# Optimization experiments

Measured on AMD Instinct MI355X. Metric: run time of the kernel, lower is better.

## Reference

```python
import jax, jax.numpy as jnp
import numpy as np

T, B, E, H, F = 1024, 2, 1024, 16, 8
D = E // H
R = 2 * T - 1  # relative positions T-1 .. -(T-1)


def setup_inputs() -> dict:
    key = jax.random.key(0)
    ks = jax.random.split(key, 11)
    std = float(np.sqrt(2.0 / (E + E)))
    return {
        "input": jax.random.normal(ks[0], (T, B, E), jnp.float32),
        "pos": jax.random.normal(ks[1], (R, B, E), jnp.float32),
        "factor": jax.random.normal(ks[2], (F,), jnp.float32),
        "in_proj_weight": jax.random.normal(ks[3], (3 * E * E, F), jnp.float32) * std,
        "pos_proj_weight": jax.random.normal(ks[4], (E * E, F), jnp.float32) * std,
        "out_proj_weight": jax.random.normal(ks[5], (E * E, F), jnp.float32) * std,
        "in_proj_bias": jax.random.normal(ks[6], (3 * E, F), jnp.float32) * 0.02,
        "pos_proj_bias": jax.random.normal(ks[7], (E, F), jnp.float32) * 0.02,
        "out_proj_bias": jax.random.normal(ks[8], (E, F), jnp.float32) * 0.02,
        "r_w_bias": jax.random.normal(ks[9], (E, F), jnp.float32) * 0.02,
        "r_r_bias": jax.random.normal(ks[10], (E, F), jnp.float32) * 0.02,
    }


def _rel_shift(x):
    # x: [BH, T, R] -> out[b, i, j] = x[b, i, j + (T-1) - i]
    bh, q, r = x.shape
    zp = jnp.zeros((bh, q, 1), x.dtype)
    xp = jnp.concatenate([zp, x], axis=2).reshape(bh, r + 1, q)
    return xp[:, 1:, :].reshape(bh, q, r)


def reference(input, pos, factor, in_proj_weight, pos_proj_weight, out_proj_weight,
              in_proj_bias, pos_proj_bias, out_proj_bias, r_w_bias, r_r_bias):
    # hypernetwork: generate effective weights from factor vector (torch.mv)
    W_in = (in_proj_weight @ factor).reshape(3 * E, E)
    W_pos = (pos_proj_weight @ factor).reshape(E, E)
    W_out = (out_proj_weight @ factor).reshape(E, E)
    b_in = in_proj_bias @ factor
    b_pos = pos_proj_bias @ factor
    b_out = out_proj_bias @ factor
    rw = (r_w_bias @ factor).reshape(H, D)  # content bias
    rr = (r_r_bias @ factor).reshape(H, D)  # position bias

    qkv = input @ W_in.T + b_in                      # [T, B, 3E]
    q, k, v = jnp.split(qkv, 3, axis=-1)
    q = q.reshape(T, B, H, D)
    k = k.reshape(T, B, H, D)
    v = v.reshape(T, B, H, D)
    r = (pos @ W_pos.T + b_pos).reshape(R, B, H, D)  # [R, B, H, D]

    scale = 1.0 / np.sqrt(D)
    # AC: content-content + content bias term
    AC = jnp.einsum('ibhd,jbhd->bhij', q + rw, k)    # [B, H, T, T]
    # BD: content-position + position bias term, then relative shift
    BD = jnp.einsum('ibhd,rbhd->bhir', q + rr, r)    # [B, H, T, R]
    BD = _rel_shift(BD.reshape(B * H, T, R))[:, :, :T].reshape(B, H, T, T)

    attn = jax.nn.softmax((AC + BD) * scale, axis=-1)  # [B, H, T, T]
    out = jnp.einsum('bhij,jbhd->ibhd', attn, v).reshape(T, B, E)
    out = out @ W_out.T + b_out                       # [T, B, E]
    return out
```

## Files before the change

kernel.cpp:

```cpp
#include <hip/hip_runtime.h>


typedef _Float16 h16;
typedef _Float16 h16x8 __attribute__((ext_vector_type(8)));
typedef _Float16 h16x4 __attribute__((ext_vector_type(4)));
typedef float f32x4 __attribute__((ext_vector_type(4)));

static __device__ __forceinline__ f32x4 mfma16(h16x8 a, h16x8 b, f32x4 c) {
  return __builtin_amdgcn_mfma_f32_16x16x32_f16(a, b, c, 0, 0, 0);
}
static __device__ __forceinline__ void gload16(const void* g, void* l) {
  __builtin_amdgcn_global_load_lds((const __attribute__((address_space(1))) void*)g,
                                   (__attribute__((address_space(3))) void*)l, 16, 0, 0);
}

__global__ __launch_bounds__(256) void hypernet_kernel(
    const float* __restrict__ fac,
    const float* __restrict__ w_in, const float* __restrict__ w_pos,
    const float* __restrict__ w_out, const float* __restrict__ b_in_w,
    const float* __restrict__ b_pos_w, const float* __restrict__ b_out_w,
    const float* __restrict__ rw_w, const float* __restrict__ rr_w,
    h16* __restrict__ Win, h16* __restrict__ Wpos, h16* __restrict__ Wout,
    float* __restrict__ bin, float* __restrict__ bpos, float* __restrict__ bout,
    float* __restrict__ rw, float* __restrict__ rr, h16* __restrict__ rb,
    const float* __restrict__ input, h16* __restrict__ in_h,
    const float* __restrict__ pos, h16* __restrict__ pos_h)
{
  float f0=fac[0],f1=fac[1],f2=fac[2],f3=fac[3],f4=fac[4],f5=fac[5],f6=fac[6],f7=fac[7];
#define DOT8(p) ((p)[0]*f0+(p)[1]*f1+(p)[2]*f2+(p)[3]*f3+(p)[4]*f4+(p)[5]*f5+(p)[6]*f6+(p)[7]*f7)
  if (blockIdx.x < 5120) {
    const int lane = threadIdx.x & 63;
    const int gw = blockIdx.x * 4 + (threadIdx.x >> 6);
    size_t rowBase = (size_t)gw * 256;
    const float* srcp; h16* dstp; size_t lr;
    if (rowBase < 3145728)      { srcp = w_in;  dstp = Win;  lr = rowBase; }
    else if (rowBase < 4194304) { srcp = w_pos; dstp = Wpos; lr = rowBase - 3145728; }
    else                        { srcp = w_out; dstp = Wout; lr = rowBase - 4194304; }
    const f32x4* p = reinterpret_cast<const f32x4*>(srcp) + lr*2;
    const int pi = (lane < 32) ? (lane << 1) : (((lane - 32) << 1) | 1);
    const float fa = (lane < 32) ? f0 : f4;
    const float fb = (lane < 32) ? f1 : f5;
    const float fc = (lane < 32) ? f2 : f6;
    const float fd = (lane < 32) ? f3 : f7;
    f32x4 v[8];
#pragma unroll
    for (int u = 0; u < 8; ++u) v[u] = p[(size_t)u*64 + pi];
    float full[8];
#pragma unroll
    for (int u = 0; u < 8; ++u) {
      float part = v[u].x*fa + v[u].y*fb + v[u].z*fc + v[u].w*fd;
      full[u] = part + __shfl_xor(part, 32, 64);
    }
    if (lane < 32) {
#pragma unroll
      for (int u = 0; u < 8; ++u)
        dstp[lr + u*32 + lane] = (h16)full[u];
    }
    return;
  }
  int idx = (blockIdx.x - 5120) * 256 + threadIdx.x;
  if (idx < 3072) { bin[idx]  = DOT8(b_in_w  + (size_t)idx*8); return; }
  idx -= 3072;
  if (idx < 1024) { bpos[idx] = DOT8(b_pos_w + (size_t)idx*8); return; }
  idx -= 1024;
  if (idx < 1024) { bout[idx] = DOT8(b_out_w + (size_t)idx*8); return; }
  idx -= 1024;
  if (idx < 1024) { rw[idx]   = DOT8(rw_w    + (size_t)idx*8); return; }
  idx -= 1024;
  if (idx < 1024) { rr[idx]   = DOT8(rr_w    + (size_t)idx*8); return; }
  idx -= 1024;
  if (idx < 2048) { rb[(((size_t)(idx >> 6)) << 17) + 2047*64 + (idx & 63)] = (h16)0.f; return; }
  idx -= 2048;
  if (idx < 262144) {
    const float4* ip = reinterpret_cast<const float4*>(input) + (size_t)idx*2;
    float4 a = ip[0], b = ip[1];
    h16x8 o = { (h16)a.x, (h16)a.y, (h16)a.z, (h16)a.w,
                (h16)b.x, (h16)b.y, (h16)b.z, (h16)b.w };
    reinterpret_cast<h16x8*>(in_h)[idx] = o;
    return;
  }
  idx -= 262144;
  if (idx < 524032) {
    const float4* pp = reinterpret_cast<const float4*>(pos) + (size_t)idx*2;
    float4 a = pp[0], b = pp[1];
    h16x8 o = { (h16)a.x, (h16)a.y, (h16)a.z, (h16)a.w,
                (h16)b.x, (h16)b.y, (h16)b.z, (h16)b.w };
    reinterpret_cast<h16x8*>(pos_h)[idx] = o;
  }
#undef DOT8
}

template <int MODE>
__global__ __launch_bounds__(256) void gemm_lds_kernel(
    const h16* __restrict__ A, const h16* __restrict__ Bw,
    const float* __restrict__ bias, int M, int N, int K,
    float* __restrict__ Cout,
    const float* __restrict__ rwv, const float* __restrict__ rrv,
    h16* __restrict__ o0, h16* __restrict__ o1,
    h16* __restrict__ o2, h16* __restrict__ o3)
{
  __shared__ __align__(16) h16 a_sm[128*64];
  __shared__ __align__(16) h16 b_sm[128*64];
  const int tid = threadIdx.x, lane = tid & 63, wave = tid >> 6;
  const int quad = lane >> 4, t16 = lane & 15;
  const int wm = wave >> 1, wn = wave & 1;
  const int m0 = blockIdx.y * 128, n0 = blockIdx.x * 128;
  const int lrow = lane >> 3, lgran = lane & 7;
  const int gsw = (lgran ^ lrow) * 8;
  const int xg0 = (quad ^ (t16 & 7)) * 8;
  const int xg1 = xg0 ^ 32;

  f32x4 acc[4][4];
#pragma unroll
  for (int i = 0; i < 4; ++i)
#pragma unroll
    for (int j = 0; j < 4; ++j) acc[i][j] = (f32x4){0.f,0.f,0.f,0.f};

  for (int k0 = 0; k0 < K; k0 += 64) {
    __syncthreads();
#pragma unroll
    for (int s = 0; s < 4; ++s) {
      int rbase = wave*32 + s*8;
      gload16(A  + (size_t)(m0 + rbase + lrow)*K + k0 + gsw, a_sm + rbase*64);
      gload16(Bw + (size_t)(n0 + rbase + lrow)*K + k0 + gsw, b_sm + rbase*64);
    }
    __syncthreads();
#pragma unroll
    for (int kc = 0; kc < 2; ++kc) {
      const int xg = kc ? xg1 : xg0;
      h16x8 af[4], bfr[4];
#pragma unroll
      for (int i = 0; i < 4; ++i) {
        af[i]  = *reinterpret_cast<const h16x8*>(a_sm + (wm*64 + i*16 + t16)*64 + xg);
        bfr[i] = *reinterpret_cast<const h16x8*>(b_sm + (wn*64 + i*16 + t16)*64 + xg);
      }
#pragma unroll
      for (int i = 0; i < 4; ++i)
#pragma unroll
        for (int j = 0; j < 4; ++j)
          acc[i][j] = mfma16(af[i], bfr[j], acc[i][j]);
    }
  }

#pragma unroll
  for (int i = 0; i < 4; ++i) {
    int mb = m0 + wm*64 + i*16 + quad*4;
#pragma unroll
    for (int j = 0; j < 4; ++j) {
      int n = n0 + wn*64 + j*16 + t16;
      float bv = bias[n];
      if (MODE == 2) {
#pragma unroll
        for (int r = 0; r < 4; ++r)
          Cout[(size_t)(mb + r)*N + n] = acc[i][j][r] + bv;
      } else if (MODE == 0) {
        int nn = n & 1023, sec = n >> 10, hh = nn >> 6, d = nn & 63;
        float rwb = rwv[nn], rrb = rrv[nn];
#pragma unroll
        for (int r = 0; r < 4; ++r) {
          int m = mb + r, t = m >> 1, b = m & 1;
          size_t off = ((size_t)((b << 4) + hh) << 16) + (t << 6) + d;
          float v = acc[i][j][r] + bv;
          if (sec == 0)      { o0[off] = (h16)(v + rwb); o1[off] = (h16)(v + rrb); }
          else if (sec == 1) { o2[off] = (h16)v; }
          else               { o3[off] = (h16)v; }
        }
      } else {
        int hh = n >> 6, d = n & 63;
#pragma unroll
        for (int r = 0; r < 4; ++r) {
          int m = mb + r;
          if (m < M) {
            int rel = m >> 1, b = m & 1;
            o0[(((size_t)((b << 4) + hh)) << 17) + (rel << 6) + d] = (h16)(acc[i][j][r] + bv);
          }
        }
      }
    }
  }
}

__global__ __launch_bounds__(256) void transpose_v_kernel(
    const h16* __restrict__ vb, h16* __restrict__ vbt)
{
  __shared__ h16 tile[64*72];
  const int bh = blockIdx.y, t0 = blockIdx.x * 64;
  const int r = threadIdx.x >> 3, c = (threadIdx.x & 7) * 8;
  const h16* src = vb + ((size_t)bh << 16) + (size_t)(t0 + r)*64 + c;
  *reinterpret_cast<h16x8*>(tile + r*72 + c)        = *reinterpret_cast<const h16x8*>(src);
  *reinterpret_cast<h16x8*>(tile + (r + 32)*72 + c) = *reinterpret_cast<const h16x8*>(src + 32*64);
  __syncthreads();
  h16x8 o0, o1;
#pragma unroll
  for (int e = 0; e < 8; ++e) {
    o0[e] = tile[(c + e)*72 + r];
    o1[e] = tile[(c + e)*72 + r + 32];
  }
  h16* dst = vbt + ((size_t)bh << 16) + (size_t)r*1024 + t0 + c;
  *reinterpret_cast<h16x8*>(dst)            = o0;
  *reinterpret_cast<h16x8*>(dst + 32*1024)  = o1;
}

__global__ __launch_bounds__(256) void flash_kernel(
    const h16* __restrict__ qrw, const h16* __restrict__ qrr,
    const h16* __restrict__ kb, const h16* __restrict__ vbt,
    const h16* __restrict__ rb,
    float* __restrict__ o_part, float* __restrict__ ml_part)
{
  __shared__ __align__(16) h16 k_sm[64*64];
  __shared__ __align__(16) h16 vt_sm[64*64];
  __shared__ __align__(16) h16 r_sm[128*64];

  const int tid = threadIdx.x, lane = tid & 63, wave = tid >> 6;
  const int quad = lane >> 4, t16 = lane & 15;
  const int bh = blockIdx.y, i0 = blockIdx.x * 64, jh = blockIdx.z;
  const size_t base  = (size_t)bh << 16;
  const size_t rbase = (size_t)bh << 17;
  const int iw = i0 + wave * 16;
  const int lrow = lane >> 3, lgran = lane & 7;
  const int gsw = (lgran ^ lrow) * 8;
  const int xg0 = (quad ^ (t16 & 7)) * 8;
  const int xg1 = xg0 ^ 32;

  h16x8 a_rw[2], a_rr[2];
  {
    const h16* p = qrw + base + (size_t)(iw + t16)*64 + quad*8;
    a_rw[0] = *reinterpret_cast<const h16x8*>(p);
    a_rw[1] = *reinterpret_cast<const h16x8*>(p + 32);
    const h16* p2 = qrr + base + (size_t)(iw + t16)*64 + quad*8;
    a_rr[0] = *reinterpret_cast<const h16x8*>(p2);
    a_rr[1] = *reinterpret_cast<const h16x8*>(p2 + 32);
  }

  f32x4 o_acc[4];
#pragma unroll
  for (int dc = 0; dc < 4; ++dc) o_acc[dc] = (f32x4){0.f,0.f,0.f,0.f};
  float m_run[4] = {-1e30f,-1e30f,-1e30f,-1e30f};
  float l_run[4] = {0.f,0.f,0.f,0.f};

  h16* bdw = r_sm + wave * (16*84);
  const int cb0 = 3 - wave;

  for (int j0 = jh*256; j0 < jh*256 + 256; j0 += 64) {
    __syncthreads();
    {
#pragma unroll
      for (int s = 0; s < 2; ++s) {
        int row = wave*16 + s*8;
        gload16(kb  + base + (size_t)(j0 + row + lrow)*64 + gsw, k_sm  + row*64);
        gload16(vbt + base + (size_t)(row + lrow)*1024 + j0 + gsw, vt_sm + row*64);
      }
      const int rel0 = j0 - i0 + 960;
#pragma unroll
      for (int s = 0; s < 4; ++s) {
        int row = wave*32 + s*8;
        gload16(rb + rbase + (size_t)(rel0 + row + lrow)*64 + gsw, r_sm + row*64);
      }
    }
    __syncthreads();

    f32x4 s_ac[4];
#pragma unroll
    for (int c = 0; c < 4; ++c) {
      s_ac[c] = (f32x4){0.f,0.f,0.f,0.f};
      s_ac[c] = mfma16(a_rw[0], *reinterpret_cast<const h16x8*>(k_sm + (c*16 + t16)*64 + xg0), s_ac[c]);
      s_ac[c] = mfma16(a_rw[1], *reinterpret_cast<const h16x8*>(k_sm + (c*16 + t16)*64 + xg1), s_ac[c]);
    }
    f32x4 s_bd[5];
#pragma unroll
    for (int u = 0; u < 5; ++u) {
      s_bd[u] = (f32x4){0.f,0.f,0.f,0.f};
      s_bd[u] = mfma16(a_rr[0], *reinterpret_cast<const h16x8*>(r_sm + ((cb0+u)*16 + t16)*64 + xg0), s_bd[u]);
      s_bd[u] = mfma16(a_rr[1], *reinterpret_cast<const h16x8*>(r_sm + ((cb0+u)*16 + t16)*64 + xg1), s_bd[u]);
    }
    __syncthreads();

#pragma unroll
    for (int u = 0; u < 5; ++u)
#pragma unroll
      for (int r = 0; r < 4; ++r)
        bdw[(quad*4 + r)*84 + u*16 + t16] = (h16)s_bd[u][r];

    float sv[4][4];
#pragma unroll
    for (int c = 0; c < 4; ++c)
#pragma unroll
      for (int r = 0; r < 4; ++r) {
        int il = quad*4 + r;
        float bdv = (float)bdw[il*84 + c*16 + t16 + 15 - il];
        sv[c][r] = (s_ac[c][r] + bdv) * 0.125f;
      }

    float alpha[4];
#pragma unroll
    for (int r = 0; r < 4; ++r) {
      float v = fmaxf(fmaxf(sv[0][r], sv[1][r]), fmaxf(sv[2][r], sv[3][r]));
#pragma unroll
      for (int off = 1; off < 16; off <<= 1) v = fmaxf(v, __shfl_xor(v, off, 64));
      float mn = fmaxf(m_run[r], v);
      alpha[r] = __expf(m_run[r] - mn);
      m_run[r] = mn;
    }
#pragma unroll
    for (int r = 0; r < 4; ++r) {
      float s0 = 0.f;
#pragma unroll
      for (int c = 0; c < 4; ++c) {
        float p = __expf(sv[c][r] - m_run[r]);
        sv[c][r] = p; s0 += p;
      }
      l_run[r] = l_run[r]*alpha[r] + s0;
    }
#pragma unroll
    for (int dc = 0; dc < 4; ++dc) {
      f32x4 t = o_acc[dc];
#pragma unroll
      for (int r = 0; r < 4; ++r) t[r] *= alpha[r];
      o_acc[dc] = t;
    }
    h16* pw = bdw;
#pragma unroll
    for (int c = 0; c < 4; ++c)
#pragma unroll
      for (int r = 0; r < 4; ++r)
        pw[(quad*4 + r)*72 + c*16 + t16] = (h16)sv[c][r];

    h16x8 ap0 = *reinterpret_cast<const h16x8*>(pw + t16*72 + quad*8);
    h16x8 ap1 = *reinterpret_cast<const h16x8*>(pw + t16*72 + 32 + quad*8);
#pragma unroll
    for (int dc = 0; dc < 4; ++dc) {
      h16x8 bv0 = *reinterpret_cast<const h16x8*>(vt_sm + (dc*16 + t16)*64 + xg0);
      h16x8 bv1 = *reinterpret_cast<const h16x8*>(vt_sm + (dc*16 + t16)*64 + xg1);
      o_acc[dc] = mfma16(ap0, bv0, o_acc[dc]);
      o_acc[dc] = mfma16(ap1, bv1, o_acc[dc]);
    }
  }

#pragma unroll
  for (int r = 0; r < 4; ++r) {
    float l = l_run[r];
#pragma unroll
    for (int off = 1; off < 16; off <<= 1) l += __shfl_xor(l, off, 64);
    l_run[r] = l;
  }
  const size_t obase = ((size_t)jh*32 + bh) * 1024 * 64;
#pragma unroll
  for (int r = 0; r < 4; ++r) {
    int i = iw + quad*4 + r;
#pragma unroll
    for (int dc = 0; dc < 4; ++dc)
      o_part[obase + (size_t)i*64 + dc*16 + t16] = o_acc[dc][r];
    if (t16 == 0) {
      size_t mo = (((size_t)jh*32 + bh)*1024 + i)*2;
      ml_part[mo]     = m_run[r];
      ml_part[mo + 1] = l_run[r];
    }
  }
}

__global__ __launch_bounds__(256) void combine_kernel(
    const float* __restrict__ o_part, const float* __restrict__ ml_part,
    h16* __restrict__ attn_h)
{
  int gid = blockIdx.x * 256 + threadIdx.x;
  int row = gid >> 4;
  int d4 = (gid & 15) * 4;
  float m[4], l[4];
#pragma unroll
  for (int p = 0; p < 4; ++p) {
    m[p] = ml_part[p*65536 + row*2];
    l[p] = ml_part[p*65536 + row*2 + 1];
  }
  float M = fmaxf(fmaxf(m[0], m[1]), fmaxf(m[2], m[3]));
  float e[4], den = 0.f;
#pragma unroll
  for (int p = 0; p < 4; ++p) { e[p] = __expf(m[p] - M); den += e[p]*l[p]; }
  float inv = 1.f / den;
  float4 acc = {0.f,0.f,0.f,0.f};
#pragma unroll
  for (int p = 0; p < 4; ++p) {
    float4 O = *reinterpret_cast<const float4*>(o_part + (size_t)p*2097152 + (size_t)row*64 + d4);
    acc.x += e[p]*O.x; acc.y += e[p]*O.y; acc.z += e[p]*O.z; acc.w += e[p]*O.w;
  }
  int bh = row >> 10, i = row & 1023, b = bh >> 4, h = bh & 15;
  h16x4 o = { (h16)(acc.x*inv), (h16)(acc.y*inv), (h16)(acc.z*inv), (h16)(acc.w*inv) };
  *reinterpret_cast<h16x4*>(attn_h + ((size_t)(i*2 + b))*1024 + h*64 + d4) = o;
}

extern "C" void kernel_launch(void* const* d_in, const int* in_sizes, int n_in,
                              void* d_out, int out_size, void* d_ws, size_t ws_size,
                              hipStream_t stream)
{
  const float* input  = (const float*)d_in[0];
  const float* pos    = (const float*)d_in[1];
  const float* fac    = (const float*)d_in[2];
  const float* w_in   = (const float*)d_in[3];
  const float* w_pos  = (const float*)d_in[4];
  const float* w_out  = (const float*)d_in[5];
  const float* bin_w  = (const float*)d_in[6];
  const float* bpos_w = (const float*)d_in[7];
  const float* bout_w = (const float*)d_in[8];
  const float* rw_w   = (const float*)d_in[9];
  const float* rr_w   = (const float*)d_in[10];
  float* out = (float*)d_out;
  (void)in_sizes; (void)n_in; (void)out_size; (void)ws_size;

  char* w = (char*)d_ws;
  auto take = [&](size_t bytes) { char* p = w; w += bytes; return p; };
  h16*   Win    = (h16*)take(3145728ull*2);
  h16*   Wpos   = (h16*)take(1048576ull*2);
  h16*   Wout   = (h16*)take(1048576ull*2);
  float* bin    = (float*)take(3072*4);
  float* bpos   = (float*)take(1024*4);
  float* bout   = (float*)take(1024*4);
  float* rw     = (float*)take(1024*4);
  float* rr     = (float*)take(1024*4);
  h16*   in_h   = (h16*)take(2097152ull*2);
  h16*   pos_h  = (h16*)take(4192256ull*2);
  h16*   qrwb   = (h16*)take(2097152ull*2);
  h16*   qrrb   = (h16*)take(2097152ull*2);
  h16*   kb     = (h16*)take(2097152ull*2);
  h16*   vb     = (h16*)take(2097152ull*2);
  h16*   vbt    = (h16*)take(2097152ull*2);
  h16*   rb     = (h16*)take(4194304ull*2);
  float* o_part = (float*)take(4ull*2097152ull*4);
  float* ml     = (float*)take(4ull*65536ull*4);
  h16*   attn_h = (h16*)take(2097152ull*2);

  hypernet_kernel<<<8227, 256, 0, stream>>>(fac, w_in, w_pos, w_out, bin_w, bpos_w, bout_w,
                                            rw_w, rr_w, Win, Wpos, Wout, bin, bpos, bout,
                                            rw, rr, rb, input, in_h, pos, pos_h);
  gemm_lds_kernel<0><<<dim3(24, 16), 256, 0, stream>>>(in_h, Win, bin, 2048, 3072, 1024,
                                                       nullptr, rw, rr, qrwb, qrrb, kb, vb);
  gemm_lds_kernel<1><<<dim3(8, 32), 256, 0, stream>>>(pos_h, Wpos, bpos, 4094, 1024, 1024,
                                                      nullptr, nullptr, nullptr, rb, nullptr, nullptr, nullptr);
  transpose_v_kernel<<<dim3(16, 32), 256, 0, stream>>>(vb, vbt);
  flash_kernel<<<dim3(16, 32, 4), 256, 0, stream>>>(qrwb, qrrb, kb, vbt, rb, o_part, ml);
  combine_kernel<<<2048, 256, 0, stream>>>(o_part, ml, attn_h);
  gemm_lds_kernel<2><<<dim3(8, 16), 256, 0, stream>>>(attn_h, Wout, bout, 2048, 1024, 1024,
                                                      out, nullptr, nullptr, nullptr, nullptr, nullptr, nullptr);
}
```

Measured before the change: 359.9 us.

## Merge QKV and position GEMMs into one launch, halve flash key splits

Folds the QKV projection and the position projection into a single grid of 640 blocks. Each block decodes its mode from a swizzled block index, which removes one launch and lets the two GEMMs share the GPU. The flash kernel now splits the key range into 2 chunks of 512 instead of 4 of 256, so the combine kernel merges only two partials and less partial output is written. A sched_barrier is also added in the hypernet kernel so all weight loads are issued before any math. Fewer key splits mean fewer flash blocks (1024), which may lower occupancy or load balance.

```diff
diff --git a/kernel.cpp b/kernel.cpp
--- a/kernel.cpp
+++ b/kernel.cpp
@@ -45,6 +45,7 @@
     f32x4 v[8];
 #pragma unroll
     for (int u = 0; u < 8; ++u) v[u] = p[(size_t)u*64 + pi];
+    __builtin_amdgcn_sched_barrier(0);
     float full[8];
 #pragma unroll
     for (int u = 0; u < 8; ++u) {
@@ -90,14 +91,106 @@
 #undef DOT8
 }
 
+__global__ __launch_bounds__(256) void gemm01_kernel(
+    const h16* __restrict__ A0, const h16* __restrict__ B0, const float* __restrict__ bias0,
+    const h16* __restrict__ A1, const h16* __restrict__ B1, const float* __restrict__ bias1,
+    const float* __restrict__ rwv, const float* __restrict__ rrv,
+    h16* __restrict__ o0, h16* __restrict__ o1,
+    h16* __restrict__ o2, h16* __restrict__ o3, h16* __restrict__ r_out)
+{
+  __shared__ __align__(16) h16 a_sm[128*64];
+  __shared__ __align__(16) h16 b_sm[128*64];
+  const int bx = blockIdx.x;
+  const int swz = (bx & 7) * 80 + (bx >> 3);
+  int mode, bxx, byy;
+  if (swz < 384) { mode = 0; bxx = swz % 24; byy = swz / 24; }
+  else           { mode = 1; int b = swz - 384; bxx = b & 7; byy = b >> 3; }
+  const h16* __restrict__ A  = mode ? A1 : A0;
+  const h16* __restrict__ Bw = mode ? B1 : B0;
+  const float* __restrict__ bias = mode ? bias1 : bias0;
+  const int M = mode ? 4094 : 2048;
+  const int K = 1024;
+
+  const int tid = threadIdx.x, lane = tid & 63, wave = tid >> 6;
+  const int quad = lane >> 4, t16 = lane & 15;
+  const int wm = wave >> 1, wn = wave & 1;
+  const int m0 = byy * 128, n0 = bxx * 128;
+  const int lrow = lane >> 3, lgran = lane & 7;
+  const int gsw = (lgran ^ lrow) * 8;
+  const int xg0 = (quad ^ (t16 & 7)) * 8;
+  const int xg1 = xg0 ^ 32;
+
+  f32x4 acc[4][4];
+#pragma unroll
+  for (int i = 0; i < 4; ++i)
+#pragma unroll
+    for (int j = 0; j < 4; ++j) acc[i][j] = (f32x4){0.f,0.f,0.f,0.f};
+
+  for (int k0 = 0; k0 < K; k0 += 64) {
+    __syncthreads();
+#pragma unroll
+    for (int s = 0; s < 4; ++s) {
+      int rbase = wave*32 + s*8;
+      gload16(A  + (size_t)(m0 + rbase + lrow)*K + k0 + gsw, a_sm + rbase*64);
+      gload16(Bw + (size_t)(n0 + rbase + lrow)*K + k0 + gsw, b_sm + rbase*64);
+    }
+    __syncthreads();
+#pragma unroll
+    for (int kc = 0; kc < 2; ++kc) {
+      const int xg = kc ? xg1 : xg0;
+      h16x8 af[4], bfr[4];
+#pragma unroll
+      for (int i = 0; i < 4; ++i) {
+        af[i]  = *reinterpret_cast<const h16x8*>(a_sm + (wm*64 + i*16 + t16)*64 + xg);
+        bfr[i] = *reinterpret_cast<const h16x8*>(b_sm + (wn*64 + i*16 + t16)*64 + xg);
+      }
+#pragma unroll
+      for (int i = 0; i < 4; ++i)
+#pragma unroll
+        for (int j = 0; j < 4; ++j)
+          acc[i][j] = mfma16(af[i], bfr[j], acc[i][j]);
+    }
+  }
+
+#pragma unroll
+  for (int i = 0; i < 4; ++i) {
+    int mb = m0 + wm*64 + i*16 + quad*4;
+#pragma unroll
+    for (int j = 0; j < 4; ++j) {
+      int n = n0 + wn*64 + j*16 + t16;
+      float bv = bias[n];
+      if (mode == 0) {
+        int nn = n & 1023, sec = n >> 10, hh = nn >> 6, d = nn & 63;
+        float rwb = rwv[nn], rrb = rrv[nn];
+#pragma unroll
+        for (int r = 0; r < 4; ++r) {
+          int m = mb + r, t = m >> 1, b = m & 1;
+          size_t off = ((size_t)((b << 4) + hh) << 16) + (t << 6) + d;
+          float v = acc[i][j][r] + bv;
+          if (sec == 0)      { o0[off] = (h16)(v + rwb); o1[off] = (h16)(v + rrb); }
+          else if (sec == 1) { o2[off] = (h16)v; }
+          else               { o3[off] = (h16)v; }
+        }
+      } else {
+        int hh = n >> 6, d = n & 63;
+#pragma unroll
+        for (int r = 0; r < 4; ++r) {
+          int m = mb + r;
+          if (m < M) {
+            int rel = m >> 1, b = m & 1;
+            r_out[(((size_t)((b << 4) + hh)) << 17) + (rel << 6) + d] = (h16)(acc[i][j][r] + bv);
+          }
+        }
+      }
+    }
+  }
+}
+
 template <int MODE>
 __global__ __launch_bounds__(256) void gemm_lds_kernel(
     const h16* __restrict__ A, const h16* __restrict__ Bw,
     const float* __restrict__ bias, int M, int N, int K,
-    float* __restrict__ Cout,
-    const float* __restrict__ rwv, const float* __restrict__ rrv,
-    h16* __restrict__ o0, h16* __restrict__ o1,
-    h16* __restrict__ o2, h16* __restrict__ o3)
+    float* __restrict__ Cout)
 {
   __shared__ __align__(16) h16 a_sm[128*64];
   __shared__ __align__(16) h16 b_sm[128*64];
@@ -149,33 +242,9 @@
     for (int j = 0; j < 4; ++j) {
       int n = n0 + wn*64 + j*16 + t16;
       float bv = bias[n];
-      if (MODE == 2) {
-#pragma unroll
-        for (int r = 0; r < 4; ++r)
-          Cout[(size_t)(mb + r)*N + n] = acc[i][j][r] + bv;
-      } else if (MODE == 0) {
-        int nn = n & 1023, sec = n >> 10, hh = nn >> 6, d = nn & 63;
-        float rwb = rwv[nn], rrb = rrv[nn];
-#pragma unroll
-        for (int r = 0; r < 4; ++r) {
-          int m = mb + r, t = m >> 1, b = m & 1;
-          size_t off = ((size_t)((b << 4) + hh) << 16) + (t << 6) + d;
-          float v = acc[i][j][r] + bv;
-          if (sec == 0)      { o0[off] = (h16)(v + rwb); o1[off] = (h16)(v + rrb); }
-          else if (sec == 1) { o2[off] = (h16)v; }
-          else               { o3[off] = (h16)v; }
-        }
-      } else {
-        int hh = n >> 6, d = n & 63;
-#pragma unroll
-        for (int r = 0; r < 4; ++r) {
-          int m = mb + r;
-          if (m < M) {
-            int rel = m >> 1, b = m & 1;
-            o0[(((size_t)((b << 4) + hh)) << 17) + (rel << 6) + d] = (h16)(acc[i][j][r] + bv);
-          }
-        }
-      }
+#pragma unroll
+      for (int r = 0; r < 4; ++r)
+        Cout[(size_t)(mb + r)*N + n] = acc[i][j][r] + bv;
     }
   }
 }
@@ -241,7 +310,7 @@
   h16* bdw = r_sm + wave * (16*84);
   const int cb0 = 3 - wave;
 
-  for (int j0 = jh*256; j0 < jh*256 + 256; j0 += 64) {
+  for (int j0 = jh*512; j0 < jh*512 + 512; j0 += 64) {
     __syncthreads();
     {
 #pragma unroll
@@ -365,20 +434,20 @@
   int gid = blockIdx.x * 256 + threadIdx.x;
   int row = gid >> 4;
   int d4 = (gid & 15) * 4;
-  float m[4], l[4];
-#pragma unroll
-  for (int p = 0; p < 4; ++p) {
+  float m[2], l[2];
+#pragma unroll
+  for (int p = 0; p < 2; ++p) {
     m[p] = ml_part[p*65536 + row*2];
     l[p] = ml_part[p*65536 + row*2 + 1];
   }
-  float M = fmaxf(fmaxf(m[0], m[1]), fmaxf(m[2], m[3]));
-  float e[4], den = 0.f;
-#pragma unroll
-  for (int p = 0; p < 4; ++p) { e[p] = __expf(m[p] - M); den += e[p]*l[p]; }
+  float M = fmaxf(m[0], m[1]);
+  float e[2], den = 0.f;
+#pragma unroll
+  for (int p = 0; p < 2; ++p) { e[p] = __expf(m[p] - M); den += e[p]*l[p]; }
   float inv = 1.f / den;
   float4 acc = {0.f,0.f,0.f,0.f};
 #pragma unroll
-  for (int p = 0; p < 4; ++p) {
+  for (int p = 0; p < 2; ++p) {
     float4 O = *reinterpret_cast<const float4*>(o_part + (size_t)p*2097152 + (size_t)row*64 + d4);
     acc.x += e[p]*O.x; acc.y += e[p]*O.y; acc.z += e[p]*O.z; acc.w += e[p]*O.w;
   }
@@ -430,13 +499,11 @@
   hypernet_kernel<<<8227, 256, 0, stream>>>(fac, w_in, w_pos, w_out, bin_w, bpos_w, bout_w,
                                             rw_w, rr_w, Win, Wpos, Wout, bin, bpos, bout,
                                             rw, rr, rb, input, in_h, pos, pos_h);
-  gemm_lds_kernel<0><<<dim3(24, 16), 256, 0, stream>>>(in_h, Win, bin, 2048, 3072, 1024,
-                                                       nullptr, rw, rr, qrwb, qrrb, kb, vb);
-  gemm_lds_kernel<1><<<dim3(8, 32), 256, 0, stream>>>(pos_h, Wpos, bpos, 4094, 1024, 1024,
-                                                      nullptr, nullptr, nullptr, rb, nullptr, nullptr, nullptr);
+  gemm01_kernel<<<640, 256, 0, stream>>>(in_h, Win, bin, pos_h, Wpos, bpos,
+                                         rw, rr, qrwb, qrrb, kb, vb, rb);
   transpose_v_kernel<<<dim3(16, 32), 256, 0, stream>>>(vb, vbt);
-  flash_kernel<<<dim3(16, 32, 4), 256, 0, stream>>>(qrwb, qrrb, kb, vbt, rb, o_part, ml);
+  flash_kernel<<<dim3(16, 32, 2), 256, 0, stream>>>(qrwb, qrrb, kb, vbt, rb, o_part, ml);
   combine_kernel<<<2048, 256, 0, stream>>>(o_part, ml, attn_h);
   gemm_lds_kernel<2><<<dim3(8, 16), 256, 0, stream>>>(attn_h, Wout, bout, 2048, 1024, 1024,
-                                                      out, nullptr, nullptr, nullptr, nullptr, nullptr, nullptr);
-}
+                                                      out);
+}
```

New measurement: 354.2 us. About the same (-1.6%).
